# Optimization experiments

Measured on AMD Instinct MI355X. Metric: run time of the kernel, lower is better.

The kernel has to match this reference:

```python
import jax, jax.numpy as jnp
import numpy as np

N_HEADS = 16
N_KV_HEADS = 4
HEAD_DIM = 128
ROPE_THETA = 1000000.0

def setup_inputs() -> dict:
    key = jax.random.key(0)
    ks = jax.random.split(key, 5)
    B, T, D = 2, 2048, 2048
    s = 1.0 / np.sqrt(D)
    return {
        'x':  jax.random.normal(ks[0], (B, T, D), dtype=jnp.float32),
        'wq': jax.random.normal(ks[1], (D, N_HEADS * HEAD_DIM), dtype=jnp.float32) * s,
        'wk': jax.random.normal(ks[2], (D, N_KV_HEADS * HEAD_DIM), dtype=jnp.float32) * s,
        'wv': jax.random.normal(ks[3], (D, N_KV_HEADS * HEAD_DIM), dtype=jnp.float32) * s,
        'wo': jax.random.normal(ks[4], (N_HEADS * HEAD_DIM, D), dtype=jnp.float32) * s,
    }

def _rope_cos_sin(T, dtype):
    # build_rope_cache: inv_freq over half the head dim, cos/sin of shape [T, HEAD_DIM]
    half = HEAD_DIM // 2
    inv_freq = 1.0 / (ROPE_THETA ** (jnp.arange(0, half, dtype=jnp.float32) * 2.0 / HEAD_DIM))
    ang = jnp.arange(T, dtype=jnp.float32)[:, None] * inv_freq[None, :]  # [T, half]
    ang = jnp.concatenate([ang, ang], axis=-1)  # [T, HEAD_DIM]
    return jnp.cos(ang).astype(dtype), jnp.sin(ang).astype(dtype)

def _rotate_half(u):
    u1, u2 = jnp.split(u, 2, axis=-1)
    return jnp.concatenate([-u2, u1], axis=-1)

def _apply_rotary(h, cos, sin):
    # h: [B, H, T, hd]; cos/sin: [T, hd]
    return h * cos[None, None, :, :] + _rotate_half(h) * sin[None, None, :, :]

def _attention(x, wq, wk, wv, wo):
    B, T, D = x.shape
    dtype = x.dtype
    scale = HEAD_DIM ** -0.5
    # QKV projection + split heads -> [B, H, T, hd]
    qh = (x @ wq).reshape(B, T, N_HEADS, HEAD_DIM).transpose(0, 2, 1, 3)
    kh = (x @ wk).reshape(B, T, N_KV_HEADS, HEAD_DIM).transpose(0, 2, 1, 3)
    vh = (x @ wv).reshape(B, T, N_KV_HEADS, HEAD_DIM).transpose(0, 2, 1, 3)
    # RoPE
    cos, sin = _rope_cos_sin(T, dtype)
    qh = _apply_rotary(qh, cos, sin)
    kh = _apply_rotary(kh, cos, sin)
    # GQA: repeat kv heads
    rep = N_HEADS // N_KV_HEADS
    kh = jnp.repeat(kh, rep, axis=1)
    vh = jnp.repeat(vh, rep, axis=1)
    # eager attention: full score matrix [B, H, T, T]
    scores = jnp.einsum('bhtd,bhsd->bhts', qh, kh) * scale
    causal = jnp.tril(jnp.ones((T, T), dtype=bool))
    neg = jnp.asarray(jnp.finfo(jnp.float32).min, dtype=jnp.float32)
    scores = jnp.where(causal[None, None, :, :], scores.astype(jnp.float32), neg)
    probs = jax.nn.softmax(scores, axis=-1).astype(dtype)
    out = jnp.einsum('bhts,bhsd->bhtd', probs, vh)
    y = out.transpose(0, 2, 1, 3).reshape(B, T, N_HEADS * HEAD_DIM)  # merge heads
    return y @ wo

def reference(x, wq, wk, wv, wo):
    return _attention(x, wq, wk, wv, wo)
```

## Files before the change

### kernel.cpp

```cpp
#include <hip/hip_runtime.h>


#define T_SZ 2048
#define D_SZ 2048
#define BT   4096

typedef __attribute__((ext_vector_type(8))) short bf16x8;
typedef __attribute__((ext_vector_type(4))) float f32x4;

__device__ __forceinline__ unsigned short f2b(float f) {
  unsigned u = __float_as_uint(f);
  u = (u + 0x7fffu + ((u >> 16) & 1u)) >> 16;
  return (unsigned short)u;
}
__device__ __forceinline__ float b2f(unsigned short h) {
  return __uint_as_float(((unsigned)h) << 16);
}

__device__ __forceinline__ void async_ld16(const void* g, void* l) {
  __builtin_amdgcn_global_load_lds(
      (const __attribute__((address_space(1))) void*)g,
      (__attribute__((address_space(3))) void*)l, 16, 0, 0);
}

union Pack8 { unsigned short us[8]; uint4 v; };

__global__ __launch_bounds__(256) void cast_f32_bf16(
    const float* __restrict__ in, unsigned short* __restrict__ out) {
  int i = (blockIdx.x * 256 + threadIdx.x) * 4;
  float4 v = *(const float4*)(in + i);
  ushort4 o;
  o.x = f2b(v.x); o.y = f2b(v.y); o.z = f2b(v.z); o.w = f2b(v.w);
  *(ushort4*)(out + i) = o;
}

__global__ __launch_bounds__(256) void cast_transpose(
    const float* __restrict__ W, unsigned short* __restrict__ WT, int K, int N) {
  __shared__ float tile[64][68];
  int n0 = blockIdx.x * 64, k0 = blockIdx.y * 64;
  int t = threadIdx.x;
#pragma unroll
  for (int i = 0; i < 4; i++) {
    int c = t + 256 * i;
    int r = c >> 4, cc = c & 15;
    float4 v = *(const float4*)(W + (size_t)(k0 + r) * N + n0 + cc * 4);
    tile[r][cc * 4 + 0] = v.x; tile[r][cc * 4 + 1] = v.y;
    tile[r][cc * 4 + 2] = v.z; tile[r][cc * 4 + 3] = v.w;
  }
  __syncthreads();
#pragma unroll
  for (int i = 0; i < 2; i++) {
    int c = t + 256 * i;
    int n = c >> 3, kc = c & 7;
    Pack8 p;
#pragma unroll
    for (int j = 0; j < 8; j++) p.us[j] = f2b(tile[kc * 8 + j][n]);
    *(uint4*)(WT + (size_t)(n0 + n) * K + k0 + kc * 8) = p.v;
  }
}

template <int OUT_BF16>
__global__ __launch_bounds__(256) void gemm_bt(
    const unsigned short* __restrict__ A, const unsigned short* __restrict__ Bt,
    void* __restrict__ C, int M, int N, int K) {
  __shared__ unsigned short As[128 * 32];
  __shared__ unsigned short Bs[128 * 32];
  int t = threadIdx.x;
  int lane = t & 63, wave = t >> 6;
  int m0 = blockIdx.y * 128, n0 = blockIdx.x * 128;
  int wm = (wave >> 1) * 64, wn = (wave & 1) * 64;
  int fr = lane & 15, fq = lane >> 4;

  int srow = wave * 32 + (lane >> 2);
  int scol = (lane & 3) * 8;
  const unsigned short* Ag = A + (size_t)(m0 + srow) * K + scol;
  const unsigned short* Bg = Bt + (size_t)(n0 + srow) * K + scol;
  unsigned short* AsW = As + wave * 1024;
  unsigned short* BsW = Bs + wave * 1024;

  f32x4 acc[4][4];
#pragma unroll
  for (int mi = 0; mi < 4; mi++)
#pragma unroll
    for (int ni = 0; ni < 4; ni++) acc[mi][ni] = (f32x4){0.f, 0.f, 0.f, 0.f};

  for (int k0 = 0; k0 < K; k0 += 32) {
    __syncthreads();
#pragma unroll
    for (int j = 0; j < 2; j++) {
      async_ld16(Ag + (size_t)j * 16 * K + k0, AsW + j * 512);
      async_ld16(Bg + (size_t)j * 16 * K + k0, BsW + j * 512);
    }
    __syncthreads();
    bf16x8 a[4], b[4];
#pragma unroll
    for (int mi = 0; mi < 4; mi++)
      a[mi] = *(const bf16x8*)(As + (wm + 16 * mi + fr) * 32 + fq * 8);
#pragma unroll
    for (int ni = 0; ni < 4; ni++)
      b[ni] = *(const bf16x8*)(Bs + (wn + 16 * ni + fr) * 32 + fq * 8);
#pragma unroll
    for (int mi = 0; mi < 4; mi++)
#pragma unroll
      for (int ni = 0; ni < 4; ni++)
        acc[mi][ni] = __builtin_amdgcn_mfma_f32_16x16x32_bf16(
            a[mi], b[ni], acc[mi][ni], 0, 0, 0);
  }
#pragma unroll
  for (int mi = 0; mi < 4; mi++)
#pragma unroll
    for (int ni = 0; ni < 4; ni++)
#pragma unroll
      for (int r = 0; r < 4; r++) {
        int row = m0 + wm + 16 * mi + fq * 4 + r;
        int col = n0 + wn + 16 * ni + fr;
        float v = acc[mi][ni][r];
        if (OUT_BF16)
          ((unsigned short*)C)[(size_t)row * N + col] = f2b(v);
        else
          ((float*)C)[(size_t)row * N + col] = v;
      }
}

template <int LOGH, int STRIDE, int SCALE_Q>
__global__ __launch_bounds__(256) void rope_inplace(unsigned short* __restrict__ X) {
  int p = blockIdx.x * 256 + threadIdx.x;
  int d = p & 63;
  int h = (p >> 6) & ((1 << LOGH) - 1);
  int row = p >> (6 + LOGH);
  int tpos = row & (T_SZ - 1);
  size_t base = (size_t)row * STRIDE + h * 128 + d;
  float u1 = b2f(X[base]), u2 = b2f(X[base + 64]);
  float inv = expf(-(float)d * 0.21586735246819178f);
  float ang = (float)tpos * inv;
  float c = cosf(ang), s = sinf(ang);
  float o1 = u1 * c - u2 * s;
  float o2 = u2 * c + u1 * s;
  if (SCALE_Q) { o1 *= 0.08838834764831845f; o2 *= 0.08838834764831845f; }
  X[base]      = f2b(o1);
  X[base + 64] = f2b(o2);
}

__global__ __launch_bounds__(256) void transpose_v(
    const unsigned short* __restrict__ V ,
    unsigned short* __restrict__ VT) {
  __shared__ unsigned short tile[64][72];
  int t0 = blockIdx.x * 64;
  int n0 = blockIdx.y * 64;
  int bk = blockIdx.z;
  int b = bk >> 2, kvh = bk & 3;
  int t = threadIdx.x;
#pragma unroll
  for (int i = 0; i < 2; i++) {
    int c = t + 256 * i;
    int r = c >> 3, cc = c & 7;
    *(uint4*)&tile[r][cc * 8] = *(const uint4*)(
        V + (size_t)(b * T_SZ + t0 + r) * 3072 + kvh * 128 + n0 + cc * 8);
  }
  __syncthreads();
#pragma unroll
  for (int i = 0; i < 2; i++) {
    int c = t + 256 * i;
    int n = c >> 3, tc = c & 7;
    Pack8 p;
#pragma unroll
    for (int j = 0; j < 8; j++) p.us[j] = tile[tc * 8 + j][n];
    *(uint4*)(VT + ((size_t)bk * 128 + n0 + n) * T_SZ + t0 + tc * 8) = p.v;
  }
}

__global__ __launch_bounds__(512) void attn(
    const unsigned short* __restrict__ Q,
    const unsigned short* __restrict__ KV,
    const unsigned short* __restrict__ VT,
    unsigned short* __restrict__ O) {
  __shared__ unsigned short Ks[2][64 * 128];
  __shared__ unsigned short Vt[128 * 64];
  __shared__ unsigned short Ps[8][16 * 76];
  int qt = blockIdx.z ? blockIdx.x : 15 - blockIdx.x;
  int h = blockIdx.y, b = blockIdx.z;
  int kvh = h >> 2;
  int t = threadIdx.x, lane = t & 63, w = t >> 6;
  int fr = lane & 15, fq = lane >> 4;
  int rsw = fr & 7;

  bf16x8 qf[4];
#pragma unroll
  for (int kk = 0; kk < 4; kk++)
    qf[kk] = *(const bf16x8*)(
        Q + (size_t)(b * T_SZ + qt * 128 + w * 16 + fr) * 3072 +
        h * 128 + kk * 32 + fq * 8);

  const unsigned short* Kg = KV + (size_t)b * T_SZ * 3072 + kvh * 128;
  const unsigned short* Vg = VT + (size_t)(b * 4 + kvh) * 128 * T_SZ;

  int k_lr = lane >> 4, k_ls = lane & 15;
  int v_lr = lane >> 3, v_ls = lane & 7;

  auto stage_k = [&](int kt_, int bf) {
#pragma unroll
    for (int j = 0; j < 2; j++) {
      int row = w * 8 + j * 4 + k_lr;
      async_ld16(Kg + (size_t)(kt_ * 64 + row) * 3072 + ((k_ls ^ (row & 7)) << 3),
                 &Ks[bf][(w * 8 + j * 4) * 128]);
    }
  };
  auto stage_v = [&](int kt_) {
#pragma unroll
    for (int j = 0; j < 2; j++) {
      int row = w * 16 + j * 8 + v_lr;
      async_ld16(Vg + (size_t)row * T_SZ + kt_ * 64 + ((v_ls ^ (row & 7)) << 3),
                 &Vt[(w * 16 + j * 8) * 64]);
    }
  };

  stage_k(0, 0);
  stage_v(0);

  {
    float tposf = (float)(qt * 128 + w * 16 + fr);
#pragma unroll
    for (int kk = 0; kk < 2; kk++)
#pragma unroll
      for (int j = 0; j < 8; j++) {
        int d = kk * 32 + (fq << 3) + j;
        float u1 = b2f((unsigned short)qf[kk][j]);
        float u2 = b2f((unsigned short)qf[kk + 2][j]);
        float inv = __expf(-(float)d * 0.21586735246819178f);
        float ang = tposf * inv, c, s;
        __sincosf(ang, &s, &c);
        qf[kk][j]     = (short)f2b((u1 * c - u2 * s) * 0.08838834764831845f);
        qf[kk + 2][j] = (short)f2b((u2 * c + u1 * s) * 0.08838834764831845f);
      }
  }

  f32x4 o[8];
#pragma unroll
  for (int i = 0; i < 8; i++) o[i] = (f32x4){0.f, 0.f, 0.f, 0.f};
  float mrow = -1e30f, lrow = 0.f;
  int qg = qt * 128 + w * 16 + fr;
  int nkt = 2 * qt + 2;

  int cur = 0;
  for (int kt = 0; kt < nkt; kt++) {
    if (kt + 1 < nkt) {
      stage_k(kt + 1, cur ^ 1);
      asm volatile("s_waitcnt vmcnt(2)" ::: "memory");
    } else {
      asm volatile("s_waitcnt vmcnt(0)" ::: "memory");
    }
    __builtin_amdgcn_s_barrier();
    asm volatile("" ::: "memory");

    const unsigned short* KsC = Ks[cur];

    f32x4 s[4];
    __builtin_amdgcn_s_setprio(1);
#pragma unroll
    for (int nn = 0; nn < 4; nn++) {
      s[nn] = (f32x4){0.f, 0.f, 0.f, 0.f};
#pragma unroll
      for (int kk = 0; kk < 4; kk++) {
        bf16x8 kf = *(const bf16x8*)(
            KsC + (nn * 16 + fr) * 128 + ((((kk << 2) + fq) ^ rsw) << 3));
        s[nn] = __builtin_amdgcn_mfma_f32_16x16x32_bf16(kf, qf[kk], s[nn], 0, 0, 0);
      }
    }
    __builtin_amdgcn_s_setprio(0);
    if (kt * 64 + 63 > qg) {
#pragma unroll
      for (int nn = 0; nn < 4; nn++)
#pragma unroll
        for (int r = 0; r < 4; r++) {
          int kvg = kt * 64 + nn * 16 + fq * 4 + r;
          if (kvg > qg) s[nn][r] = -1e30f;
        }
    }
    f32x4 t4;
#pragma unroll
    for (int r = 0; r < 4; r++)
      t4[r] = fmaxf(fmaxf(s[0][r], s[1][r]), fmaxf(s[2][r], s[3][r]));
    float mx = fmaxf(fmaxf(t4[0], t4[1]), fmaxf(t4[2], t4[3]));
    mx = fmaxf(mx, __shfl_xor(mx, 16, 64));
    mx = fmaxf(mx, __shfl_xor(mx, 32, 64));
    float mnew = fmaxf(mrow, mx);
    float sum = 0.f;
#pragma unroll
    for (int nn = 0; nn < 4; nn++) {
      ushort4 pk;
      float p0 = __expf(s[nn][0] - mnew); pk.x = f2b(p0);
      float p1 = __expf(s[nn][1] - mnew); pk.y = f2b(p1);
      float p2 = __expf(s[nn][2] - mnew); pk.z = f2b(p2);
      float p3 = __expf(s[nn][3] - mnew); pk.w = f2b(p3);
      sum += (p0 + p1) + (p2 + p3);
      *(ushort4*)(Ps[w] + fr * 76 + nn * 16 + fq * 4) = pk;
    }
    float alpha = __expf(mrow - mnew);
    lrow = lrow * alpha + sum;
    mrow = mnew;
#pragma unroll
    for (int nt = 0; nt < 8; nt++)
#pragma unroll
      for (int r = 0; r < 4; r++) o[nt][r] *= alpha;
    __builtin_amdgcn_s_setprio(1);
#pragma unroll
    for (int kk = 0; kk < 2; kk++) {
      bf16x8 pf = *(const bf16x8*)(Ps[w] + fr * 76 + kk * 32 + fq * 8);
#pragma unroll
      for (int nt = 0; nt < 8; nt++) {
        bf16x8 vf = *(const bf16x8*)(
            Vt + (nt * 16 + fr) * 64 + ((((kk << 2) + fq) ^ rsw) << 3));
        o[nt] = __builtin_amdgcn_mfma_f32_16x16x32_bf16(vf, pf, o[nt], 0, 0, 0);
      }
    }
    __builtin_amdgcn_s_setprio(0);
    asm volatile("s_waitcnt lgkmcnt(0)" ::: "memory");
    __builtin_amdgcn_s_barrier();
    asm volatile("" ::: "memory");
    if (kt + 1 < nkt) stage_v(kt + 1);
    cur ^= 1;
  }
  float lsum = lrow;
  lsum += __shfl_xor(lsum, 16, 64);
  lsum += __shfl_xor(lsum, 32, 64);
  float linv = 1.f / lsum;
  int rowg = b * T_SZ + qt * 128 + w * 16 + fr;
#pragma unroll
  for (int nt = 0; nt < 8; nt++) {
    ushort4 ov;
    ov.x = f2b(o[nt][0] * linv);
    ov.y = f2b(o[nt][1] * linv);
    ov.z = f2b(o[nt][2] * linv);
    ov.w = f2b(o[nt][3] * linv);
    *(ushort4*)(O + (size_t)rowg * 2048 + h * 128 + nt * 16 + fq * 4) = ov;
  }
}

extern "C" void kernel_launch(void* const* d_in, const int* in_sizes, int n_in,
                              void* d_out, int out_size, void* d_ws, size_t ws_size,
                              hipStream_t stream) {
  const float* x  = (const float*)d_in[0];
  const float* wq = (const float*)d_in[1];
  const float* wk = (const float*)d_in[2];
  const float* wv = (const float*)d_in[3];
  const float* wo = (const float*)d_in[4];
  float* out = (float*)d_out;

  unsigned short* xb   = (unsigned short*)d_ws;
  unsigned short* wqT  = xb   + (size_t)4096 * 2048;
  unsigned short* wkT  = wqT  + (size_t)2048 * 2048;
  unsigned short* wvT  = wkT  + (size_t)512 * 2048;
  unsigned short* woT  = wvT  + (size_t)512 * 2048;
  unsigned short* QKVb = woT  + (size_t)2048 * 2048;
  unsigned short* VTb  = QKVb + (size_t)4096 * 3072;
  unsigned short* AOb  = VTb  + (size_t)4096 * 512;

  cast_f32_bf16<<<8192, 256, 0, stream>>>(x, xb);
  cast_transpose<<<dim3(32, 32), 256, 0, stream>>>(wq, wqT, 2048, 2048);
  cast_transpose<<<dim3(8, 32),  256, 0, stream>>>(wk, wkT, 2048, 512);
  cast_transpose<<<dim3(8, 32),  256, 0, stream>>>(wv, wvT, 2048, 512);
  cast_transpose<<<dim3(32, 32), 256, 0, stream>>>(wo, woT, 2048, 2048);

  gemm_bt<1><<<dim3(24, 32), 256, 0, stream>>>(xb, wqT, QKVb, 4096, 3072, 2048);

  rope_inplace<2, 3072, 0><<<4096, 256, 0, stream>>>(QKVb + 2048);
  transpose_v<<<dim3(32, 2, 8), 256, 0, stream>>>(QKVb + 2560, VTb);

  attn<<<dim3(16, 16, 2), 512, 0, stream>>>(QKVb, QKVb + 2048, VTb, AOb);

  gemm_bt<0><<<dim3(16, 32), 256, 0, stream>>>(AOb, woT, (void*)out, 4096, 2048, 2048);
}
```

Baseline: 326.1 us.

## Double-buffer GEMM loads, use exp2 lazy-rescale softmax, merge weight cast kernels

```diff
diff --git a/kernel.cpp b/kernel.cpp
--- a/kernel.cpp
+++ b/kernel.cpp
@@ -16,6 +16,14 @@
 __device__ __forceinline__ float b2f(unsigned short h) {
   return __uint_as_float(((unsigned)h) << 16);
 }
+
+#if __has_builtin(__builtin_amdgcn_exp2f)
+__device__ __forceinline__ float exp2_fast(float x) { return __builtin_amdgcn_exp2f(x); }
+#else
+__device__ __forceinline__ float exp2_fast(float x) {
+  float r; asm("v_exp_f32 %0, %1" : "=v"(r) : "v"(x)); return r;
+}
+#endif
 
 __device__ __forceinline__ void async_ld16(const void* g, void* l) {
   __builtin_amdgcn_global_load_lds(
@@ -34,10 +42,19 @@
   *(ushort4*)(out + i) = o;
 }
 
-__global__ __launch_bounds__(256) void cast_transpose(
-    const float* __restrict__ W, unsigned short* __restrict__ WT, int K, int N) {
+__global__ __launch_bounds__(256) void cast_transpose_all(
+    const float* __restrict__ wq, const float* __restrict__ wk,
+    const float* __restrict__ wv, const float* __restrict__ wo,
+    unsigned short* __restrict__ qkvT, unsigned short* __restrict__ woT) {
   __shared__ float tile[64][68];
-  int n0 = blockIdx.x * 64, k0 = blockIdx.y * 64;
+  int bx = blockIdx.x;
+  const float* W; unsigned short* WT; int N, nb;
+  if (bx < 32)      { W = wq; WT = qkvT;                         N = 2048; nb = bx; }
+  else if (bx < 40) { W = wk; WT = qkvT + (size_t)2048 * 2048;   N = 512;  nb = bx - 32; }
+  else if (bx < 48) { W = wv; WT = qkvT + (size_t)2560 * 2048;   N = 512;  nb = bx - 40; }
+  else              { W = wo; WT = woT;                          N = 2048; nb = bx - 48; }
+  const int K = 2048;
+  int n0 = nb * 64, k0 = blockIdx.y * 64;
   int t = threadIdx.x;
 #pragma unroll
   for (int i = 0; i < 4; i++) {
@@ -63,8 +80,8 @@
 __global__ __launch_bounds__(256) void gemm_bt(
     const unsigned short* __restrict__ A, const unsigned short* __restrict__ Bt,
     void* __restrict__ C, int M, int N, int K) {
-  __shared__ unsigned short As[128 * 32];
-  __shared__ unsigned short Bs[128 * 32];
+  __shared__ unsigned short As[2][128 * 32];
+  __shared__ unsigned short Bs[2][128 * 32];
   int t = threadIdx.x;
   int lane = t & 63, wave = t >> 6;
   int m0 = blockIdx.y * 128, n0 = blockIdx.x * 128;
@@ -75,8 +92,14 @@
   int scol = (lane & 3) * 8;
   const unsigned short* Ag = A + (size_t)(m0 + srow) * K + scol;
   const unsigned short* Bg = Bt + (size_t)(n0 + srow) * K + scol;
-  unsigned short* AsW = As + wave * 1024;
-  unsigned short* BsW = Bs + wave * 1024;
+
+  auto stage = [&](int k0_, int bf) {
+#pragma unroll
+    for (int j = 0; j < 2; j++) {
+      async_ld16(Ag + (size_t)j * 16 * K + k0_, &As[bf][wave * 1024 + j * 512]);
+      async_ld16(Bg + (size_t)j * 16 * K + k0_, &Bs[bf][wave * 1024 + j * 512]);
+    }
+  };
 
   f32x4 acc[4][4];
 #pragma unroll
@@ -84,27 +107,34 @@
 #pragma unroll
     for (int ni = 0; ni < 4; ni++) acc[mi][ni] = (f32x4){0.f, 0.f, 0.f, 0.f};
 
+  stage(0, 0);
+  int cur = 0;
   for (int k0 = 0; k0 < K; k0 += 32) {
-    __syncthreads();
-#pragma unroll
-    for (int j = 0; j < 2; j++) {
-      async_ld16(Ag + (size_t)j * 16 * K + k0, AsW + j * 512);
-      async_ld16(Bg + (size_t)j * 16 * K + k0, BsW + j * 512);
-    }
-    __syncthreads();
+    if (k0 + 32 < K) {
+      stage(k0 + 32, cur ^ 1);
+      asm volatile("s_waitcnt vmcnt(4)" ::: "memory");
+    } else {
+      asm volatile("s_waitcnt vmcnt(0)" ::: "memory");
+    }
+    __builtin_amdgcn_s_barrier();
+    asm volatile("" ::: "memory");
     bf16x8 a[4], b[4];
 #pragma unroll
     for (int mi = 0; mi < 4; mi++)
-      a[mi] = *(const bf16x8*)(As + (wm + 16 * mi + fr) * 32 + fq * 8);
+      a[mi] = *(const bf16x8*)(&As[cur][(wm + 16 * mi + fr) * 32 + fq * 8]);
 #pragma unroll
     for (int ni = 0; ni < 4; ni++)
-      b[ni] = *(const bf16x8*)(Bs + (wn + 16 * ni + fr) * 32 + fq * 8);
+      b[ni] = *(const bf16x8*)(&Bs[cur][(wn + 16 * ni + fr) * 32 + fq * 8]);
 #pragma unroll
     for (int mi = 0; mi < 4; mi++)
 #pragma unroll
       for (int ni = 0; ni < 4; ni++)
         acc[mi][ni] = __builtin_amdgcn_mfma_f32_16x16x32_bf16(
             a[mi], b[ni], acc[mi][ni], 0, 0, 0);
+    asm volatile("s_waitcnt lgkmcnt(0)" ::: "memory");
+    __builtin_amdgcn_s_barrier();
+    asm volatile("" ::: "memory");
+    cur ^= 1;
   }
 #pragma unroll
   for (int mi = 0; mi < 4; mi++)
@@ -218,6 +248,7 @@
   stage_v(0);
 
   {
+    const float QSCL = 0.08838834764831845f * 1.4426950408889634f;
     float tposf = (float)(qt * 128 + w * 16 + fr);
 #pragma unroll
     for (int kk = 0; kk < 2; kk++)
@@ -229,8 +260,8 @@
         float inv = __expf(-(float)d * 0.21586735246819178f);
         float ang = tposf * inv, c, s;
         __sincosf(ang, &s, &c);
-        qf[kk][j]     = (short)f2b((u1 * c - u2 * s) * 0.08838834764831845f);
-        qf[kk + 2][j] = (short)f2b((u2 * c + u1 * s) * 0.08838834764831845f);
+        qf[kk][j]     = (short)f2b((u1 * c - u2 * s) * QSCL);
+        qf[kk + 2][j] = (short)f2b((u2 * c + u1 * s) * QSCL);
       }
   }
 
@@ -283,25 +314,28 @@
     float mx = fmaxf(fmaxf(t4[0], t4[1]), fmaxf(t4[2], t4[3]));
     mx = fmaxf(mx, __shfl_xor(mx, 16, 64));
     mx = fmaxf(mx, __shfl_xor(mx, 32, 64));
-    float mnew = fmaxf(mrow, mx);
+    if (__any(mx > mrow + 8.0f)) {
+      float mnew = fmaxf(mrow, mx);
+      float alpha = exp2_fast(mrow - mnew);
+      lrow *= alpha;
+#pragma unroll
+      for (int nt = 0; nt < 8; nt++)
+#pragma unroll
+        for (int r = 0; r < 4; r++) o[nt][r] *= alpha;
+      mrow = mnew;
+    }
     float sum = 0.f;
 #pragma unroll
     for (int nn = 0; nn < 4; nn++) {
       ushort4 pk;
-      float p0 = __expf(s[nn][0] - mnew); pk.x = f2b(p0);
-      float p1 = __expf(s[nn][1] - mnew); pk.y = f2b(p1);
-      float p2 = __expf(s[nn][2] - mnew); pk.z = f2b(p2);
-      float p3 = __expf(s[nn][3] - mnew); pk.w = f2b(p3);
+      float p0 = exp2_fast(s[nn][0] - mrow); pk.x = f2b(p0);
+      float p1 = exp2_fast(s[nn][1] - mrow); pk.y = f2b(p1);
+      float p2 = exp2_fast(s[nn][2] - mrow); pk.z = f2b(p2);
+      float p3 = exp2_fast(s[nn][3] - mrow); pk.w = f2b(p3);
       sum += (p0 + p1) + (p2 + p3);
       *(ushort4*)(Ps[w] + fr * 76 + nn * 16 + fq * 4) = pk;
     }
-    float alpha = __expf(mrow - mnew);
-    lrow = lrow * alpha + sum;
-    mrow = mnew;
-#pragma unroll
-    for (int nt = 0; nt < 8; nt++)
-#pragma unroll
-      for (int r = 0; r < 4; r++) o[nt][r] *= alpha;
+    lrow += sum;
     __builtin_amdgcn_s_setprio(1);
 #pragma unroll
     for (int kk = 0; kk < 2; kk++) {
@@ -348,18 +382,13 @@
 
   unsigned short* xb   = (unsigned short*)d_ws;
   unsigned short* wqT  = xb   + (size_t)4096 * 2048;
-  unsigned short* wkT  = wqT  + (size_t)2048 * 2048;
-  unsigned short* wvT  = wkT  + (size_t)512 * 2048;
-  unsigned short* woT  = wvT  + (size_t)512 * 2048;
+  unsigned short* woT  = wqT  + (size_t)3072 * 2048;
   unsigned short* QKVb = woT  + (size_t)2048 * 2048;
   unsigned short* VTb  = QKVb + (size_t)4096 * 3072;
   unsigned short* AOb  = VTb  + (size_t)4096 * 512;
 
   cast_f32_bf16<<<8192, 256, 0, stream>>>(x, xb);
-  cast_transpose<<<dim3(32, 32), 256, 0, stream>>>(wq, wqT, 2048, 2048);
-  cast_transpose<<<dim3(8, 32),  256, 0, stream>>>(wk, wkT, 2048, 512);
-  cast_transpose<<<dim3(8, 32),  256, 0, stream>>>(wv, wvT, 2048, 512);
-  cast_transpose<<<dim3(32, 32), 256, 0, stream>>>(wo, woT, 2048, 2048);
+  cast_transpose_all<<<dim3(80, 32), 256, 0, stream>>>(wq, wk, wv, wo, wqT, woT);
 
   gemm_bt<1><<<dim3(24, 32), 256, 0, stream>>>(xb, wqT, QKVb, 4096, 3072, 2048);
 
```

After: 299.5 us. 1.09x faster.
